# Optimization experiments

Measured on AMD Instinct MI355X. Metric: run time of the kernel, lower is better.

The kernel has to match this reference:

```python
import jax, jax.numpy as jnp
import numpy as np

B, S, DIM = 2, 2048, 1024
H, W = 16, 256
HD = DIM // H
SCALE = HD ** -0.5


def setup_inputs() -> dict:
    key = jax.random.key(0)
    ks = jax.random.split(key, 9)
    std = DIM ** -0.5
    return {
        "x": jax.random.normal(ks[0], (B, S, DIM), dtype=jnp.float32),
        "Wq": jax.random.normal(ks[1], (DIM, DIM), dtype=jnp.float32) * std,
        "bq": jnp.zeros((DIM,), dtype=jnp.float32),
        "Wk": jax.random.normal(ks[2], (DIM, DIM), dtype=jnp.float32) * std,
        "bk": jnp.zeros((DIM,), dtype=jnp.float32),
        "Wv": jax.random.normal(ks[3], (DIM, DIM), dtype=jnp.float32) * std,
        "bv": jnp.zeros((DIM,), dtype=jnp.float32),
        "Wo": jax.random.normal(ks[4], (DIM, DIM), dtype=jnp.float32) * std,
        "bo": jnp.zeros((DIM,), dtype=jnp.float32),
    }


def reference(x, Wq, bq, Wk, bk, Wv, bv, Wo, bo):
    b, s, dim = x.shape
    q = (x @ Wq + bq).reshape(b, s, H, HD).transpose(0, 2, 1, 3)  # [B,H,S,HD]
    k = (x @ Wk + bk).reshape(b, s, H, HD).transpose(0, 2, 1, 3)
    v = (x @ Wv + bv).reshape(b, s, H, HD).transpose(0, 2, 1, 3)

    scores = jnp.einsum("bhid,bhjd->bhij", q, k) * SCALE  # [B,H,S,S]
    i = jnp.arange(s)[:, None]
    j = jnp.arange(s)[None, :]
    # valid keys: within causal sliding window [i-W+1, i]
    valid = (j <= i) & (j >= i - W + 1)
    scores = jnp.where(valid, scores, -jnp.inf)
    attn = jax.nn.softmax(scores, axis=-1)
    out = jnp.einsum("bhij,bhjd->bhid", attn, v)  # [B,H,S,HD]
    out = out.transpose(0, 2, 1, 3).reshape(b, s, dim)
    return out @ Wo + bo
```

## Files before the change

### kernel.cpp

```cpp
#include <hip/hip_runtime.h>
#include <stdint.h>

typedef __bf16 bf16;
typedef __bf16 bf16x8 __attribute__((ext_vector_type(8)));
typedef float f32x4 __attribute__((ext_vector_type(4)));

#define MFMA16(a, b, c) __builtin_amdgcn_mfma_f32_16x16x32_bf16((a), (b), (c), 0, 0, 0)

__device__ __forceinline__ void ldsdma16(const void* g, void* l) {
  __builtin_amdgcn_global_load_lds((const __attribute__((address_space(1))) void*)g,
                                   (__attribute__((address_space(3))) void*)l, 16, 0, 0);
}

__global__ __launch_bounds__(256) void prep_kernel(const float* __restrict__ x,
                                                   const float* __restrict__ Wq,
                                                   const float* __restrict__ Wk,
                                                   const float* __restrict__ Wv,
                                                   const float* __restrict__ Wo,
                                                   bf16* __restrict__ xb,
                                                   bf16* __restrict__ WT) {
  __shared__ float tile[64][65];
  if (blockIdx.z == 4) {
    const int t = (blockIdx.y * 16 + blockIdx.x) * 256 + threadIdx.x;
#pragma unroll
    for (int i = 0; i < 16; ++i) {
      const int idx = (t + i * 65536) * 4;
      float4 v = *(const float4*)(x + idx);
      union { bf16 h[4]; uint2 u; } p;
      p.h[0] = (bf16)v.x; p.h[1] = (bf16)v.y; p.h[2] = (bf16)v.z; p.h[3] = (bf16)v.w;
      *(uint2*)(xb + idx) = p.u;
    }
    return;
  }
  const float* src = blockIdx.z == 0 ? Wq : blockIdx.z == 1 ? Wk : blockIdx.z == 2 ? Wv : Wo;
  bf16* dst = WT + (size_t)blockIdx.z * 1024 * 1024;
  const int k0 = blockIdx.y * 64, n0 = blockIdx.x * 64;
  const int rr = threadIdx.x >> 6, c = threadIdx.x & 63;
#pragma unroll
  for (int i = 0; i < 16; ++i) {
    int r = i * 4 + rr;
    tile[r][c] = src[(size_t)(k0 + r) * 1024 + n0 + c];
  }
  __syncthreads();
#pragma unroll
  for (int i = 0; i < 16; ++i) {
    int r = i * 4 + rr;
    dst[(size_t)(n0 + r) * 1024 + k0 + c] = (bf16)tile[c][r];
  }
}

__device__ __forceinline__ void stage_half(const bf16* __restrict__ src, int rowbase,
                                           int koff, char* lds, int bufq, int wave,
                                           int lane) {
#pragma unroll
  for (int i = 0; i < 2; ++i) {
    int chunk = i * 512 + wave * 64 + lane;
    int row = chunk >> 3;
    int cg = (chunk & 7) ^ (row & 7);
    ldsdma16(src + (size_t)(rowbase + row) * 1024 + koff + cg * 8,
             lds + bufq * 16384 + (i * 512 + wave * 64) * 16);
  }
}

__device__ __forceinline__ void ld_frag4(const bf16* lds, int bufq, int rbase, int quad,
                                         int l16, bf16x8 (&d)[4][2]) {
  const bf16x8* hb = (const bf16x8*)lds + bufq * 1024;
#pragma unroll
  for (int mf = 0; mf < 4; ++mf) {
    int row = rbase + mf * 16 + l16;
#pragma unroll
    for (int kk = 0; kk < 2; ++kk)
      d[mf][kk] = hb[row * 8 + ((kk * 4 + quad) ^ (row & 7))];
  }
}

__device__ __forceinline__ void ld_frag2(const bf16* lds, int bufq, int rbase, int quad,
                                         int l16, bf16x8 (&d)[2][2]) {
  const bf16x8* hb = (const bf16x8*)lds + bufq * 1024;
#pragma unroll
  for (int nf = 0; nf < 2; ++nf) {
    int row = rbase + nf * 16 + l16;
#pragma unroll
    for (int kk = 0; kk < 2; ++kk)
      d[nf][kk] = hb[row * 8 + ((kk * 4 + quad) ^ (row & 7))];
  }
}

template <int MQ, int NQ>
__device__ __forceinline__ void mma_quad(f32x4 (&acc)[8][4], const bf16x8 (&a)[4][2],
                                         const bf16x8 (&b)[2][2]) {
  __builtin_amdgcn_s_setprio(1);
#pragma unroll
  for (int mf = 0; mf < 4; ++mf)
#pragma unroll
    for (int nf = 0; nf < 2; ++nf)
#pragma unroll
      for (int kk = 0; kk < 2; ++kk)
        acc[MQ * 4 + mf][NQ * 2 + nf] =
            MFMA16(a[mf][kk], b[nf][kk], acc[MQ * 4 + mf][NQ * 2 + nf]);
  __builtin_amdgcn_s_setprio(0);
}

#define QBAR1() { __builtin_amdgcn_s_barrier(); \
                  asm volatile("s_waitcnt lgkmcnt(0)" ::: "memory"); }
#define QBAR2() { __builtin_amdgcn_s_barrier(); }

template <bool PRE>
__device__ __forceinline__ void qkv_iter(int k0, const bf16* __restrict__ xb,
                                         const bf16* __restrict__ BT, int m0, int n0,
                                         bf16* As, bf16* Bs, f32x4 (&acc)[8][4], int wave,
                                         int lane, int wm, int wn, int quad, int l16) {
  bf16x8 aF[4][2], b0F[2][2], b1F[2][2];
  ld_frag4(As, 0, wm * 64, quad, l16, aF);
  ld_frag2(Bs, 0, wn * 32, quad, l16, b0F);
  stage_half(xb, m0 + 128, k0 + 64, (char*)As, 3, wave, lane);
  QBAR1(); mma_quad<0, 0>(acc, aF, b0F); QBAR2();
  ld_frag2(Bs, 1, wn * 32, quad, l16, b1F);
  stage_half(BT, n0, k0 + 64, (char*)Bs, 2, wave, lane);
  QBAR1(); mma_quad<0, 1>(acc, aF, b1F); QBAR2();
  ld_frag4(As, 1, wm * 64, quad, l16, aF);
  if (PRE) stage_half(xb, m0, k0 + 128, (char*)As, 0, wave, lane);
  QBAR1(); mma_quad<1, 1>(acc, aF, b1F); QBAR2();
  if (PRE) stage_half(BT, n0 + 128, k0 + 128, (char*)Bs, 1, wave, lane);
  QBAR1(); mma_quad<1, 0>(acc, aF, b0F);
  if (PRE) { asm volatile("s_waitcnt vmcnt(4)" ::: "memory"); }
  else     { asm volatile("s_waitcnt vmcnt(0)" ::: "memory"); }
  QBAR2();
  ld_frag4(As, 2, wm * 64, quad, l16, aF);
  ld_frag2(Bs, 2, wn * 32, quad, l16, b0F);
  if (PRE) stage_half(xb, m0 + 128, k0 + 128, (char*)As, 1, wave, lane);
  QBAR1(); mma_quad<0, 0>(acc, aF, b0F); QBAR2();
  ld_frag2(Bs, 3, wn * 32, quad, l16, b1F);
  if (PRE) stage_half(BT, n0, k0 + 128, (char*)Bs, 0, wave, lane);
  QBAR1(); mma_quad<0, 1>(acc, aF, b1F); QBAR2();
  ld_frag4(As, 3, wm * 64, quad, l16, aF);
  if (PRE) stage_half(xb, m0, k0 + 192, (char*)As, 2, wave, lane);
  QBAR1(); mma_quad<1, 1>(acc, aF, b1F); QBAR2();
  if (PRE) stage_half(BT, n0 + 128, k0 + 192, (char*)Bs, 3, wave, lane);
  QBAR1(); mma_quad<1, 0>(acc, aF, b0F);
  if (PRE) { asm volatile("s_waitcnt vmcnt(4)" ::: "memory"); }
  QBAR2();
}

__global__ __launch_bounds__(512) void qkv_gemm8(const bf16* __restrict__ xb,
                                                 const bf16* __restrict__ WT,
                                                 const float* __restrict__ bq,
                                                 const float* __restrict__ bk,
                                                 const float* __restrict__ bv,
                                                 bf16* __restrict__ Qd,
                                                 bf16* __restrict__ Kd,
                                                 bf16* __restrict__ Vd) {
  extern __shared__ char smem_raw[];
  bf16* As = (bf16*)smem_raw;
  bf16* Bs = (bf16*)(smem_raw + 65536);

  const int tid = threadIdx.x, lane = tid & 63, wave = tid >> 6;
  const int wm = wave >> 2, wn = wave & 3;
  const int quad = lane >> 4, l16 = lane & 15;
  const int ob = (blockIdx.x & 7) * 24 + (blockIdx.x >> 3);
  const int m0 = (ob / 12) * 256, n0 = (ob % 12) * 256;

  f32x4 acc[8][4];
  const f32x4 zero = {0.f, 0.f, 0.f, 0.f};
#pragma unroll
  for (int i = 0; i < 8; ++i)
#pragma unroll
    for (int j = 0; j < 4; ++j) acc[i][j] = zero;

  stage_half(xb, m0, 0, (char*)As, 0, wave, lane);
  stage_half(WT, n0, 0, (char*)Bs, 0, wave, lane);
  stage_half(xb, m0 + 128, 0, (char*)As, 1, wave, lane);
  stage_half(WT, n0 + 128, 0, (char*)Bs, 1, wave, lane);
  stage_half(xb, m0, 64, (char*)As, 2, wave, lane);
  stage_half(WT, n0 + 128, 64, (char*)Bs, 3, wave, lane);
  asm volatile("s_waitcnt vmcnt(4)" ::: "memory");
  __builtin_amdgcn_s_barrier();

  for (int j = 0; j < 7; ++j)
    qkv_iter<true>(j * 128, xb, WT, m0, n0, As, Bs, acc, wave, lane, wm, wn, quad, l16);
  qkv_iter<false>(896, xb, WT, m0, n0, As, Bs, acc, wave, lane, wm, wn, quad, l16);

#pragma unroll
  for (int MQ = 0; MQ < 2; ++MQ)
#pragma unroll
    for (int mf = 0; mf < 4; ++mf)
#pragma unroll
      for (int NQ = 0; NQ < 2; ++NQ)
#pragma unroll
        for (int nf = 0; nf < 2; ++nf) {
          const int n = n0 + NQ * 128 + wn * 32 + nf * 16 + l16;
          const int sel = n >> 10, d = n & 1023;
          const float bias = (sel == 0 ? bq : sel == 1 ? bk : bv)[d];
          bf16* dst = (sel == 0 ? Qd : sel == 1 ? Kd : Vd);
          const float scl = (sel == 0) ? 0.125f : 1.f;
          const int h = d >> 6, hd = d & 63;
#pragma unroll
          for (int r = 0; r < 4; ++r) {
            const int token = m0 + MQ * 128 + wm * 64 + mf * 16 + quad * 4 + r;
            const int bb = token >> 11, s = token & 2047;
            const float v = (acc[MQ * 4 + mf][NQ * 2 + nf][r] + bias) * scl;
            dst[((((size_t)bb * 16 + h) * 2048 + s) << 6) + hd] = (bf16)v;
          }
        }
}

template <int NJ>
__device__ __forceinline__ void gemm_mainloop(const bf16* __restrict__ A,
                                              const bf16* __restrict__ BT, int K,
                                              int m0, int n0, bf16* As, bf16* Bs,
                                              f32x4 (&acc)[4][NJ]) {
  constexpr int BN = NJ * 32;
  const int tid = threadIdx.x;
  const int lane = tid & 63;
  const int wave = tid >> 6;
  const int wm = wave >> 1, wn = wave & 1;
  const int quad = lane >> 4, l16 = lane & 15;

  const f32x4 zero = {0.f, 0.f, 0.f, 0.f};
#pragma unroll
  for (int i = 0; i < 4; ++i)
#pragma unroll
    for (int j = 0; j < NJ; ++j) acc[i][j] = zero;

  for (int k0 = 0; k0 < K; k0 += 32) {
#pragma unroll
    for (int c = 0; c < 2; ++c) {
      int chunk = wave * 128 + c * 64 + lane;
      int row = chunk >> 2;
      int cg = (chunk & 3) ^ ((row >> 1) & 3);
      ldsdma16(A + (size_t)(m0 + row) * K + k0 + cg * 8,
               (char*)As + (size_t)(wave * 128 + c * 64) * 16);
    }
#pragma unroll
    for (int c = 0; c < BN / 64; ++c) {
      int chunk = wave * (BN / 64) * 64 + c * 64 + lane;
      int row = chunk >> 2;
      int cg = (chunk & 3) ^ ((row >> 1) & 3);
      ldsdma16(BT + (size_t)(n0 + row) * K + k0 + cg * 8,
               (char*)Bs + (size_t)(wave * (BN / 64) * 64 + c * 64) * 16);
    }
    __syncthreads();
    bf16x8 af[4], bfv[NJ];
#pragma unroll
    for (int i = 0; i < 4; ++i) {
      int ra = wm * 64 + i * 16 + l16;
      af[i] = ((const bf16x8*)As)[ra * 4 + (quad ^ ((ra >> 1) & 3))];
    }
#pragma unroll
    for (int j = 0; j < NJ; ++j) {
      int rb = wn * (BN / 2) + j * 16 + l16;
      bfv[j] = ((const bf16x8*)Bs)[rb * 4 + (quad ^ ((rb >> 1) & 3))];
    }
#pragma unroll
    for (int i = 0; i < 4; ++i)
#pragma unroll
      for (int j = 0; j < NJ; ++j) acc[i][j] = MFMA16(af[i], bfv[j], acc[i][j]);
    __syncthreads();
  }
}

template <int NT, int MODE>
__device__ __forceinline__ void attn_phase(const int start, const bf16* __restrict__ Kb,
                                           const bf16* __restrict__ Vb, bf16* KsPs, bf16* Vt,
                                           const bf16x8 qa0, const bf16x8 qa1,
                                           const int i0, float (&mrow)[4], float (&lrow)[4],
                                           f32x4 (&oacc)[4]) {
  const int tid = threadIdx.x, lane = tid & 63, wave = tid >> 6;
  const int quad = lane >> 4, l16 = lane & 15;
  const f32x4 zero = {0.f, 0.f, 0.f, 0.f};

  __syncthreads();
#pragma unroll
  for (int c = 0; c < NT / 2; ++c) {
    int chunk = c * 256 + wave * 64 + lane;
    int row = chunk >> 3;
    int cg = (chunk & 7) ^ (row & 7);
    ldsdma16(Kb + (size_t)(start + row) * 64 + cg * 8,
             (char*)KsPs + (size_t)(c * 256 + wave * 64) * 16);
  }
  if (NT == 8) {
    const int key = tid >> 1, hc = (tid & 1) * 32;
    const bf16* vp = Vb + (size_t)(start + key) * 64 + hc;
    bf16x8 v0 = ((const bf16x8*)vp)[0], v1 = ((const bf16x8*)vp)[1];
    bf16x8 v2 = ((const bf16x8*)vp)[2], v3 = ((const bf16x8*)vp)[3];
#pragma unroll
    for (int i = 0; i < 8; ++i) Vt[(hc + i) * 136 + key] = v0[i];
#pragma unroll
    for (int i = 0; i < 8; ++i) Vt[(hc + 8 + i) * 136 + key] = v1[i];
#pragma unroll
    for (int i = 0; i < 8; ++i) Vt[(hc + 16 + i) * 136 + key] = v2[i];
#pragma unroll
    for (int i = 0; i < 8; ++i) Vt[(hc + 24 + i) * 136 + key] = v3[i];
  } else {
    const int key = tid >> 2, hc = (tid & 3) * 16;
    const bf16* vp = Vb + (size_t)(start + key) * 64 + hc;
    bf16x8 v0 = ((const bf16x8*)vp)[0], v1 = ((const bf16x8*)vp)[1];
#pragma unroll
    for (int i = 0; i < 8; ++i) Vt[(hc + i) * 136 + key] = v0[i];
#pragma unroll
    for (int i = 0; i < 8; ++i) Vt[(hc + 8 + i) * 136 + key] = v1[i];
  }
  __syncthreads();

  f32x4 sc[NT];
  __builtin_amdgcn_s_setprio(1);
#pragma unroll
  for (int nt = 0; nt < NT; ++nt) {
    int key = nt * 16 + l16;
    bf16x8 kb0 = ((const bf16x8*)KsPs)[key * 8 + ((0 * 4 + quad) ^ (key & 7))];
    bf16x8 kb1 = ((const bf16x8*)KsPs)[key * 8 + ((1 * 4 + quad) ^ (key & 7))];
    f32x4 s = zero;
    s = MFMA16(qa0, kb0, s);
    s = MFMA16(qa1, kb1, s);
    sc[nt] = s;
  }
  __builtin_amdgcn_s_setprio(0);

  float alpha[4];
#pragma unroll
  for (int r = 0; r < 4; ++r) {
    const int i = i0 + r;
    float mx = -1e30f;
#pragma unroll
    for (int nt = 0; nt < NT; ++nt) {
      float s = sc[nt][r];
      if (MODE == 1) {
        const bool valid = (start + nt * 16 + l16 + 255 >= i);
        s = valid ? s : -1e30f;
        sc[nt][r] = s;
      } else if (MODE == 2) {
        const bool valid = (start + nt * 16 + l16 <= i);
        s = valid ? s : -1e30f;
        sc[nt][r] = s;
      }
      mx = fmaxf(mx, s);
    }
#pragma unroll
    for (int m = 8; m >= 1; m >>= 1) mx = fmaxf(mx, __shfl_xor(mx, m, 64));
    const float mnew = fmaxf(mrow[r], mx);
    alpha[r] = __expf(mrow[r] - mnew);
    mrow[r] = mnew;
    float rs = 0.f;
#pragma unroll
    for (int nt = 0; nt < NT; ++nt) {
      const float p = __expf(sc[nt][r] - mnew);
      sc[nt][r] = p;
      rs += p;
    }
#pragma unroll
    for (int m = 8; m >= 1; m >>= 1) rs += __shfl_xor(rs, m, 64);
    lrow[r] = lrow[r] * alpha[r] + rs;
  }

  __builtin_amdgcn_s_barrier();

  bf16* Psw = KsPs + wave * (16 * 136);
#pragma unroll
  for (int nt = 0; nt < NT; ++nt)
#pragma unroll
    for (int r = 0; r < 4; ++r)
      Psw[(quad * 4 + r) * 136 + nt * 16 + l16] = (bf16)sc[nt][r];
  asm volatile("s_waitcnt lgkmcnt(0)" ::: "memory");
  bf16x8 pa[NT / 2];
#pragma unroll
  for (int ks = 0; ks < NT / 2; ++ks)
    pa[ks] = ((const bf16x8*)Psw)[l16 * 17 + ks * 4 + quad];

  __builtin_amdgcn_s_setprio(1);
#pragma unroll
  for (int ht = 0; ht < 4; ++ht) {
    f32x4 o = oacc[ht];
#pragma unroll
    for (int r = 0; r < 4; ++r) o[r] *= alpha[r];
#pragma unroll
    for (int ks = 0; ks < NT / 2; ++ks) {
      bf16x8 vb = ((const bf16x8*)Vt)[(ht * 16 + l16) * 17 + ks * 4 + quad];
      o = MFMA16(pa[ks], vb, o);
    }
    oacc[ht] = o;
  }
  __builtin_amdgcn_s_setprio(0);
}

__global__ __launch_bounds__(256, 4) void attn_kernel(const bf16* __restrict__ Q,
                                                      const bf16* __restrict__ K,
                                                      const bf16* __restrict__ V,
                                                      bf16* __restrict__ Ao) {
  __shared__ bf16 KsPs[8704] __attribute__((aligned(16)));
  __shared__ bf16 Vt[64 * 136] __attribute__((aligned(16)));

  const int tid = threadIdx.x, lane = tid & 63, wave = tid >> 6;
  const int quad = lane >> 4, l16 = lane & 15;
  const int ob = (blockIdx.x & 7) * 128 + (blockIdx.x >> 3);
  const int qt = ob & 31, h = (ob >> 5) & 15, b = ob >> 9;
  const int q0 = qt * 64;
  const size_t base = ((size_t)(b * 16 + h)) * 2048 * 64;
  const bf16* Qb = Q + base + (size_t)q0 * 64;
  const bf16* Kb = K + base;
  const bf16* Vb = V + base;

  const bf16* qrow = Qb + (size_t)(wave * 16 + l16) * 64 + quad * 8;
  const bf16x8 qa0 = *(const bf16x8*)qrow;
  const bf16x8 qa1 = *(const bf16x8*)(qrow + 32);

  float mrow[4], lrow[4];
  f32x4 oacc[4];
  const f32x4 zero = {0.f, 0.f, 0.f, 0.f};
#pragma unroll
  for (int r = 0; r < 4; ++r) { mrow[r] = -1e30f; lrow[r] = 0.f; }
#pragma unroll
  for (int t = 0; t < 4; ++t) oacc[t] = zero;

  const int i0 = q0 + wave * 16 + quad * 4;

  if (q0 >= 256)
    attn_phase<8, 1>(q0 - 256, Kb, Vb, KsPs, Vt, qa0, qa1, i0, mrow, lrow, oacc);
  else if (q0 == 192)
    attn_phase<4, 0>(0, Kb, Vb, KsPs, Vt, qa0, qa1, i0, mrow, lrow, oacc);
  if (q0 >= 128)
    attn_phase<8, 0>(q0 - 128, Kb, Vb, KsPs, Vt, qa0, qa1, i0, mrow, lrow, oacc);
  else if (q0 == 64)
    attn_phase<4, 0>(0, Kb, Vb, KsPs, Vt, qa0, qa1, i0, mrow, lrow, oacc);
  attn_phase<4, 2>(q0, Kb, Vb, KsPs, Vt, qa0, qa1, i0, mrow, lrow, oacc);

#pragma unroll
  for (int r = 0; r < 4; ++r) {
    const float inv = 1.f / lrow[r];
    const int row = q0 + wave * 16 + quad * 4 + r;
    const size_t outb = ((size_t)(b * 2048 + row)) * 1024 + h * 64;
#pragma unroll
    for (int ht = 0; ht < 4; ++ht)
      Ao[outb + ht * 16 + l16] = (bf16)(oacc[ht][r] * inv);
  }
}

__global__ __launch_bounds__(256) void out_gemm(const bf16* __restrict__ Ain,
                                                const bf16* __restrict__ WoT,
                                                const float* __restrict__ bo,
                                                float* __restrict__ out) {
  __shared__ bf16 As[128 * 32] __attribute__((aligned(16)));
  __shared__ bf16 Bs[64 * 32] __attribute__((aligned(16)));
  f32x4 acc[4][2];
  const int ob = (blockIdx.x & 7) * 64 + (blockIdx.x >> 3);
  const int m0 = (ob >> 4) * 128, n0 = (ob & 15) * 64;
  gemm_mainloop<2>(Ain, WoT, 1024, m0, n0, As, Bs, acc);

  const int lane = threadIdx.x & 63, wave = threadIdx.x >> 6;
  const int wm = wave >> 1, wn = wave & 1;
  const int quad = lane >> 4, l16 = lane & 15;
#pragma unroll
  for (int j = 0; j < 2; ++j) {
    const int n = n0 + wn * 32 + j * 16 + l16;
    const float bias = bo[n];
#pragma unroll
    for (int i = 0; i < 4; ++i) {
#pragma unroll
      for (int r = 0; r < 4; ++r) {
        const int token = m0 + wm * 64 + i * 16 + quad * 4 + r;
        out[(size_t)token * 1024 + n] = acc[i][j][r] + bias;
      }
    }
  }
}

extern "C" void kernel_launch(void* const* d_in, const int* in_sizes, int n_in,
                              void* d_out, int out_size, void* d_ws, size_t ws_size,
                              hipStream_t stream) {
  const float* x  = (const float*)d_in[0];
  const float* Wq = (const float*)d_in[1];
  const float* bq = (const float*)d_in[2];
  const float* Wk = (const float*)d_in[3];
  const float* bk = (const float*)d_in[4];
  const float* Wv = (const float*)d_in[5];
  const float* bv = (const float*)d_in[6];
  const float* Wo = (const float*)d_in[7];
  const float* bo = (const float*)d_in[8];
  float* out = (float*)d_out;

  char* ws = (char*)d_ws;
  bf16* xb = (bf16*)(ws);
  bf16* WT = (bf16*)(ws + ((size_t)8 << 20));
  bf16* Qd = (bf16*)(ws + ((size_t)16 << 20));
  bf16* Kd = (bf16*)(ws + ((size_t)24 << 20));
  bf16* Vd = (bf16*)(ws + ((size_t)32 << 20));
  bf16* Ao = (bf16*)(ws + ((size_t)40 << 20));

  (void)hipFuncSetAttribute((const void*)qkv_gemm8,
                            hipFuncAttributeMaxDynamicSharedMemorySize, 131072);

  prep_kernel<<<dim3(16, 16, 5), 256, 0, stream>>>(x, Wq, Wk, Wv, Wo, xb, WT);
  qkv_gemm8<<<dim3(192), 512, 131072, stream>>>(xb, WT, bq, bk, bv, Qd, Kd, Vd);
  attn_kernel<<<dim3(1024), 256, 0, stream>>>(Qd, Kd, Vd, Ao);
  out_gemm<<<dim3(512), 256, 0, stream>>>(Ao, WT + (size_t)3 * 1024 * 1024, bo, out);
}
```

Baseline: 164.4 us.

## Use 128-query, 8-wave attention blocks to share K/V tiles across more queries

```diff
diff --git a/kernel.cpp b/kernel.cpp
--- a/kernel.cpp
+++ b/kernel.cpp
@@ -259,39 +259,26 @@
   }
 }
 
-template <int NT, int MODE>
-__device__ __forceinline__ void attn_phase(const int start, const bf16* __restrict__ Kb,
-                                           const bf16* __restrict__ Vb, bf16* KsPs, bf16* Vt,
-                                           const bf16x8 qa0, const bf16x8 qa1,
-                                           const int i0, float (&mrow)[4], float (&lrow)[4],
-                                           f32x4 (&oacc)[4]) {
+template <int MODE>
+__device__ __forceinline__ void attn_phase8w(const int start, const bf16* __restrict__ Kb,
+                                             const bf16* __restrict__ Vb, bf16* KsPs,
+                                             bf16* Vt, const bf16x8 qa0, const bf16x8 qa1,
+                                             const int i0, float (&mrow)[4],
+                                             float (&lrow)[4], f32x4 (&oacc)[4]) {
   const int tid = threadIdx.x, lane = tid & 63, wave = tid >> 6;
   const int quad = lane >> 4, l16 = lane & 15;
   const f32x4 zero = {0.f, 0.f, 0.f, 0.f};
 
   __syncthreads();
 #pragma unroll
-  for (int c = 0; c < NT / 2; ++c) {
-    int chunk = c * 256 + wave * 64 + lane;
+  for (int c = 0; c < 2; ++c) {
+    int chunk = c * 512 + wave * 64 + lane;
     int row = chunk >> 3;
     int cg = (chunk & 7) ^ (row & 7);
     ldsdma16(Kb + (size_t)(start + row) * 64 + cg * 8,
-             (char*)KsPs + (size_t)(c * 256 + wave * 64) * 16);
-  }
-  if (NT == 8) {
-    const int key = tid >> 1, hc = (tid & 1) * 32;
-    const bf16* vp = Vb + (size_t)(start + key) * 64 + hc;
-    bf16x8 v0 = ((const bf16x8*)vp)[0], v1 = ((const bf16x8*)vp)[1];
-    bf16x8 v2 = ((const bf16x8*)vp)[2], v3 = ((const bf16x8*)vp)[3];
-#pragma unroll
-    for (int i = 0; i < 8; ++i) Vt[(hc + i) * 136 + key] = v0[i];
-#pragma unroll
-    for (int i = 0; i < 8; ++i) Vt[(hc + 8 + i) * 136 + key] = v1[i];
-#pragma unroll
-    for (int i = 0; i < 8; ++i) Vt[(hc + 16 + i) * 136 + key] = v2[i];
-#pragma unroll
-    for (int i = 0; i < 8; ++i) Vt[(hc + 24 + i) * 136 + key] = v3[i];
-  } else {
+             (char*)KsPs + (size_t)(c * 512 + wave * 64) * 16);
+  }
+  {
     const int key = tid >> 2, hc = (tid & 3) * 16;
     const bf16* vp = Vb + (size_t)(start + key) * 64 + hc;
     bf16x8 v0 = ((const bf16x8*)vp)[0], v1 = ((const bf16x8*)vp)[1];
@@ -302,10 +289,10 @@
   }
   __syncthreads();
 
-  f32x4 sc[NT];
+  f32x4 sc[8];
   __builtin_amdgcn_s_setprio(1);
 #pragma unroll
-  for (int nt = 0; nt < NT; ++nt) {
+  for (int nt = 0; nt < 8; ++nt) {
     int key = nt * 16 + l16;
     bf16x8 kb0 = ((const bf16x8*)KsPs)[key * 8 + ((0 * 4 + quad) ^ (key & 7))];
     bf16x8 kb1 = ((const bf16x8*)KsPs)[key * 8 + ((1 * 4 + quad) ^ (key & 7))];
@@ -322,7 +309,7 @@
     const int i = i0 + r;
     float mx = -1e30f;
 #pragma unroll
-    for (int nt = 0; nt < NT; ++nt) {
+    for (int nt = 0; nt < 8; ++nt) {
       float s = sc[nt][r];
       if (MODE == 1) {
         const bool valid = (start + nt * 16 + l16 + 255 >= i);
@@ -342,7 +329,7 @@
     mrow[r] = mnew;
     float rs = 0.f;
 #pragma unroll
-    for (int nt = 0; nt < NT; ++nt) {
+    for (int nt = 0; nt < 8; ++nt) {
       const float p = __expf(sc[nt][r] - mnew);
       sc[nt][r] = p;
       rs += p;
@@ -356,14 +343,14 @@
 
   bf16* Psw = KsPs + wave * (16 * 136);
 #pragma unroll
-  for (int nt = 0; nt < NT; ++nt)
+  for (int nt = 0; nt < 8; ++nt)
 #pragma unroll
     for (int r = 0; r < 4; ++r)
       Psw[(quad * 4 + r) * 136 + nt * 16 + l16] = (bf16)sc[nt][r];
   asm volatile("s_waitcnt lgkmcnt(0)" ::: "memory");
-  bf16x8 pa[NT / 2];
-#pragma unroll
-  for (int ks = 0; ks < NT / 2; ++ks)
+  bf16x8 pa[4];
+#pragma unroll
+  for (int ks = 0; ks < 4; ++ks)
     pa[ks] = ((const bf16x8*)Psw)[l16 * 17 + ks * 4 + quad];
 
   __builtin_amdgcn_s_setprio(1);
@@ -373,7 +360,7 @@
 #pragma unroll
     for (int r = 0; r < 4; ++r) o[r] *= alpha[r];
 #pragma unroll
-    for (int ks = 0; ks < NT / 2; ++ks) {
+    for (int ks = 0; ks < 4; ++ks) {
       bf16x8 vb = ((const bf16x8*)Vt)[(ht * 16 + l16) * 17 + ks * 4 + quad];
       o = MFMA16(pa[ks], vb, o);
     }
@@ -382,18 +369,18 @@
   __builtin_amdgcn_s_setprio(0);
 }
 
-__global__ __launch_bounds__(256, 4) void attn_kernel(const bf16* __restrict__ Q,
-                                                      const bf16* __restrict__ K,
-                                                      const bf16* __restrict__ V,
-                                                      bf16* __restrict__ Ao) {
-  __shared__ bf16 KsPs[8704] __attribute__((aligned(16)));
+__global__ __launch_bounds__(512) void attn_kernel(const bf16* __restrict__ Q,
+                                                   const bf16* __restrict__ K,
+                                                   const bf16* __restrict__ V,
+                                                   bf16* __restrict__ Ao) {
+  __shared__ bf16 KsPs[17408] __attribute__((aligned(16)));
   __shared__ bf16 Vt[64 * 136] __attribute__((aligned(16)));
 
   const int tid = threadIdx.x, lane = tid & 63, wave = tid >> 6;
   const int quad = lane >> 4, l16 = lane & 15;
-  const int ob = (blockIdx.x & 7) * 128 + (blockIdx.x >> 3);
-  const int qt = ob & 31, h = (ob >> 5) & 15, b = ob >> 9;
-  const int q0 = qt * 64;
+  const int ob = (blockIdx.x & 7) * 64 + (blockIdx.x >> 3);
+  const int qt = ob & 15, h = (ob >> 4) & 15, b = ob >> 8;
+  const int q0 = qt * 128;
   const size_t base = ((size_t)(b * 16 + h)) * 2048 * 64;
   const bf16* Qb = Q + base + (size_t)q0 * 64;
   const bf16* Kb = K + base;
@@ -414,14 +401,10 @@
   const int i0 = q0 + wave * 16 + quad * 4;
 
   if (q0 >= 256)
-    attn_phase<8, 1>(q0 - 256, Kb, Vb, KsPs, Vt, qa0, qa1, i0, mrow, lrow, oacc);
-  else if (q0 == 192)
-    attn_phase<4, 0>(0, Kb, Vb, KsPs, Vt, qa0, qa1, i0, mrow, lrow, oacc);
+    attn_phase8w<1>(q0 - 256, Kb, Vb, KsPs, Vt, qa0, qa1, i0, mrow, lrow, oacc);
   if (q0 >= 128)
-    attn_phase<8, 0>(q0 - 128, Kb, Vb, KsPs, Vt, qa0, qa1, i0, mrow, lrow, oacc);
-  else if (q0 == 64)
-    attn_phase<4, 0>(0, Kb, Vb, KsPs, Vt, qa0, qa1, i0, mrow, lrow, oacc);
-  attn_phase<4, 2>(q0, Kb, Vb, KsPs, Vt, qa0, qa1, i0, mrow, lrow, oacc);
+    attn_phase8w<0>(q0 - 128, Kb, Vb, KsPs, Vt, qa0, qa1, i0, mrow, lrow, oacc);
+  attn_phase8w<2>(q0, Kb, Vb, KsPs, Vt, qa0, qa1, i0, mrow, lrow, oacc);
 
 #pragma unroll
   for (int r = 0; r < 4; ++r) {
@@ -490,6 +473,6 @@
 
   prep_kernel<<<dim3(16, 16, 5), 256, 0, stream>>>(x, Wq, Wk, Wv, Wo, xb, WT);
   qkv_gemm8<<<dim3(192), 512, 131072, stream>>>(xb, WT, bq, bk, bv, Qd, Kd, Vd);
-  attn_kernel<<<dim3(1024), 256, 0, stream>>>(Qd, Kd, Vd, Ao);
+  attn_kernel<<<dim3(512), 512, 0, stream>>>(Qd, Kd, Vd, Ao);
   out_gemm<<<dim3(512), 256, 0, stream>>>(Ao, WT + (size_t)3 * 1024 * 1024, bo, out);
 }
```

Result: slower. 170.4 us (+3.7%).
